# Kernel optimization log

Measured on AMD Instinct MI355X. Metric: run time of the kernel, lower is better.

The kernel has to match this reference:

```python
import jax, jax.numpy as jnp
import numpy as np

T, B, IN_DIM, H = 512, 64, 1024, 1024

def setup_inputs() -> dict:
    key = jax.random.key(0)
    kx, kwx, kwh = jax.random.split(key, 3)
    x = jax.random.normal(kx, (T, B, IN_DIM), dtype=jnp.float32)
    # lecun_normal: std = 1/sqrt(fan_in)
    W_x = jax.random.normal(kwx, (IN_DIM, 4 * H), dtype=jnp.float32) / np.sqrt(IN_DIM)
    W_h = jax.random.normal(kwh, (H, 4 * H), dtype=jnp.float32) / np.sqrt(H)
    b = jnp.zeros((4 * H,), dtype=jnp.float32)
    return {"x": x, "W_x": W_x, "W_h": W_h, "b": b}

def reference(x, W_x, W_h, b):
    Tn, Bn, _ = x.shape
    Hn = W_h.shape[0]
    h0 = jnp.zeros((Bn, Hn), dtype=x.dtype)
    c0 = jnp.zeros((Bn, Hn), dtype=x.dtype)

    def step(carry, xt):
        h, c = carry
        gates = xt @ W_x + h @ W_h + b  # [B, 4H]
        i, f, g, o = jnp.split(gates, 4, axis=-1)
        i = jax.nn.sigmoid(i)
        f = jax.nn.sigmoid(f)
        o = jax.nn.sigmoid(o)
        g = jnp.tanh(g)
        c_new = f * c + i * g
        h_new = o * jnp.tanh(c_new)
        return (h_new, c_new), h_new

    (hT, cT), hs = jax.lax.scan(step, (h0, c0), x)
    return hs, (hT, cT)
```

## Files before the change

kernel.cpp:

```cpp
#include <hip/hip_runtime.h>

typedef unsigned short u16;
typedef unsigned int u32;
typedef unsigned long long u64;
typedef float f32x4 __attribute__((ext_vector_type(4)));
typedef __bf16 bf16x8 __attribute__((ext_vector_type(8)));
typedef u16 u16x8 __attribute__((ext_vector_type(8)));
typedef u32 u32x4 __attribute__((ext_vector_type(4)));

#define T_STEPS 512
#define BATCH 64
#define HDIM 1024
#define GDIM 4096
#define HS_ELEMS (33554432u)
#define XP_STEP 262144

__device__ __forceinline__ u16 f2bf(float f) {
  union { float f; u32 u; } v; v.f = f;
  u32 r = v.u + 0x7fffu + ((v.u >> 16) & 1u);
  return (u16)(r >> 16);
}
__device__ __forceinline__ float bf2f(u16 b) {
  union { u32 u; float f; } v; v.u = ((u32)b) << 16;
  return v.f;
}
__device__ __forceinline__ float sigm(float x) { return 1.f / (1.f + __expf(-x)); }
__device__ __forceinline__ float tanh_fast(float x) { return 1.f - 2.f / (__expf(2.f * x) + 1.f); }

__device__ __forceinline__ void gload16(const void* g, void* l) {
  __builtin_amdgcn_global_load_lds(
      (const __attribute__((address_space(1))) u32*)g,
      (__attribute__((address_space(3))) u32*)l, 16, 0, 0);
}
__device__ __forceinline__ u32x4 cload16(const void* g) {
  u32x4 r;
  asm volatile("global_load_dwordx4 %0, %1, off sc0 sc1" : "=&v"(r) : "v"(g) : "memory");
  return r;
}

__global__ void transpose_w(const float* __restrict__ Wx, const float* __restrict__ Wh,
                            u16* __restrict__ WxT, u16* __restrict__ WhT) {
  __shared__ float tile[32][33];
  const float* src = blockIdx.z ? Wh : Wx;
  u16* dst = blockIdx.z ? WhT : WxT;
  const int n0 = blockIdx.x * 32, k0 = blockIdx.y * 32;
  const int tx = threadIdx.x, ty = threadIdx.y;
#pragma unroll
  for (int i = 0; i < 4; ++i)
    tile[ty + i * 8][tx] = src[(size_t)(k0 + ty + i * 8) * GDIM + n0 + tx];
  __syncthreads();
#pragma unroll
  for (int i = 0; i < 4; ++i)
    dst[(size_t)(n0 + ty + i * 8) * HDIM + k0 + tx] = f2bf(tile[tx][ty + i * 8]);
}

__global__ void convert_x(const float* __restrict__ X, u16* __restrict__ Xbf) {
  const size_t i = ((size_t)blockIdx.x * 256 + threadIdx.x) * 8;
  const float4 a = *(const float4*)&X[i];
  const float4 b = *(const float4*)&X[i + 4];
  u16x8 o;
  o[0] = f2bf(a.x); o[1] = f2bf(a.y); o[2] = f2bf(a.z); o[3] = f2bf(a.w);
  o[4] = f2bf(b.x); o[5] = f2bf(b.y); o[6] = f2bf(b.z); o[7] = f2bf(b.w);
  *(u16x8*)&Xbf[i] = o;
}

__global__ __launch_bounds__(256) void gemm_xp(
    const u16* __restrict__ Xbf, const u16* __restrict__ WxT,
    const float* __restrict__ bias, u16* __restrict__ Xp) {
  __shared__ u16 As[128 * 32];
  __shared__ u16 Bs[128 * 32];
  const int tid = threadIdx.x;
  const int lane = tid & 63, w = tid >> 6;
  const int rl = lane & 15, gq = lane >> 4, g8 = gq * 8;
  const int swz = (blockIdx.x & 7) * 1024 + (blockIdx.x >> 3);
  const int m0 = (swz >> 5) * 128, n0 = (swz & 31) * 128;
  const int rbase = (w >> 1) * 64, cbase = (w & 1) * 64;
  const int r0 = tid >> 2, c0 = (tid & 3) * 8;

  f32x4 acc[4][4] = {};
  for (int k0 = 0; k0 < 1024; k0 += 32) {
    gload16(&Xbf[(size_t)(m0 + r0) * 1024 + k0 + c0], &As[w * 512]);
    gload16(&Xbf[(size_t)(m0 + r0 + 64) * 1024 + k0 + c0], &As[2048 + w * 512]);
    gload16(&WxT[(size_t)(n0 + r0) * 1024 + k0 + c0], &Bs[w * 512]);
    gload16(&WxT[(size_t)(n0 + r0 + 64) * 1024 + k0 + c0], &Bs[2048 + w * 512]);
    __syncthreads();
    bf16x8 av[4], bv[4];
#pragma unroll
    for (int i = 0; i < 4; ++i)
      av[i] = *(const bf16x8*)&As[(rbase + i * 16 + rl) * 32 + g8];
#pragma unroll
    for (int j = 0; j < 4; ++j)
      bv[j] = *(const bf16x8*)&Bs[(cbase + j * 16 + rl) * 32 + g8];
#pragma unroll
    for (int i = 0; i < 4; ++i)
#pragma unroll
      for (int j = 0; j < 4; ++j)
        acc[i][j] = __builtin_amdgcn_mfma_f32_16x16x32_bf16(av[i], bv[j], acc[i][j], 0, 0, 0);
    __syncthreads();
  }
#pragma unroll
  for (int j = 0; j < 4; ++j) {
    const int n = n0 + cbase + j * 16 + rl;
    const float bj = bias[n];
    const int gate = n >> 10, col = n & 1023;
    const int cri = col >> 5, hcoli = col & 31;
#pragma unroll
    for (int i = 0; i < 4; ++i)
#pragma unroll
      for (int r = 0; r < 4; ++r) {
        const int m = m0 + rbase + i * 16 + gq * 4 + r;
        const int tt = m >> 6, b = m & 63;
        Xp[(size_t)tt * XP_STEP + (size_t)((b >> 4) * 32 + cri) * 2048 +
           gate * 512 + (b & 15) * 32 + hcoli] = f2bf(acc[i][j][r] + bj);
      }
  }
}

__global__ void zero_tags(u32* __restrict__ ht) {
  const u32 i = blockIdx.x * 256 + threadIdx.x;
  if (i < 131200u) ht[i] = 0;
}

__global__ __launch_bounds__(512, 1) void lstm_rec(
    const u16* __restrict__ Xp, const u16* __restrict__ WhT,
    u32* __restrict__ h_tag, u32* __restrict__ flags, float* __restrict__ out) {
  __shared__ u16 h_lds[16 * 1024];
  __shared__ float gate_lds[4][2][16][20];
  const int tid = threadIdx.x;
  const int lane = tid & 63, w = tid >> 6;
  const int rl = lane & 15, gq = lane >> 4;
  const int cr = blockIdx.x & 31, bg = blockIdx.x >> 5;
  const int g = w >> 1, c2 = w & 1;

  bf16x8 wf[32];
  {
    const size_t gcol = (size_t)(g * 1024 + cr * 32 + c2 * 16 + rl) * HDIM + gq * 8;
#pragma unroll
    for (int kk = 0; kk < 32; ++kk)
      wf[kk] = *(const bf16x8*)&WhT[gcol + kk * 32];
  }

  const int b_el = tid >> 5, hcol = tid & 31;
  const int srow = tid >> 5, s32 = tid & 31;
  const int swz_w = ((srow & 7) << 4) ^ ((srow & 1) << 6);
  const int swz_r = ((rl & 7) << 4) ^ ((rl & 1) << 6);
  float creg = 0.f, hreg = 0.f;

  const u16* xp_p = Xp + (size_t)blockIdx.x * 2048 + tid;
  float xg0 = bf2f(xp_p[0]), xg1 = bf2f(xp_p[512]),
        xg2 = bf2f(xp_p[1024]), xg3 = bf2f(xp_p[1536]);

  const u32* flagrow = flags + bg * 32 + (lane & 31);

  for (int t = 0; t < T_STEPS; ++t) {
    u16 nx0 = 0, nx1 = 0, nx2 = 0, nx3 = 0;
    if (t + 1 < T_STEPS) {
      const u16* p = xp_p + XP_STEP;
      nx0 = p[0]; nx1 = p[512]; nx2 = p[1024]; nx3 = p[1536];
    }

    f32x4 acc0 = {0.f, 0.f, 0.f, 0.f}, acc1 = {0.f, 0.f, 0.f, 0.f};
    if (t > 0) {
      const u32* hrow32 =
          h_tag + (size_t)(t & 1) * 65536 + (size_t)(bg * 16 + srow) * 1024;
      char* ldsrow = (char*)h_lds + srow * 2048;
      u32x4 v[8];
#pragma unroll
      for (int u = 0; u < 8; ++u)
        v[u] = cload16((const char*)hrow32 + 512 * u + 16 * s32);
      asm volatile("s_waitcnt vmcnt(0)" ::: "memory");
      __builtin_amdgcn_sched_barrier(0);
      u32 pend = 0u;
#pragma unroll
      for (int u = 0; u < 8; ++u) {
        const u32 w0 = v[u][0], w1 = v[u][1], w2 = v[u][2], w3 = v[u][3];
        const u64 packs = (u64)((w0 & 0xffffu) | (w1 << 16)) |
                          ((u64)((w2 & 0xffffu) | (w3 << 16)) << 32);
        *(u64*)(ldsrow + ((256 * u + 8 * s32) ^ swz_w)) = packs;
        if ((w0 >> 16) < (u32)t || (w1 >> 16) < (u32)t ||
            (w2 >> 16) < (u32)t || (w3 >> 16) < (u32)t)
          pend |= (1u << u);
      }
      if (__builtin_expect(pend != 0u, 0)) {
        for (;;) {
          u32 f = __hip_atomic_load(flagrow, __ATOMIC_RELAXED, __HIP_MEMORY_SCOPE_AGENT);
          if (__all((int)(f >= (u32)t))) break;
        }
        u32x4 r[8];
#pragma unroll
        for (int u = 0; u < 8; ++u)
          if (pend & (1u << u))
            r[u] = cload16((const char*)hrow32 + 512 * u + 16 * s32);
        asm volatile("s_waitcnt vmcnt(0)" ::: "memory");
        __builtin_amdgcn_sched_barrier(0);
#pragma unroll
        for (int u = 0; u < 8; ++u)
          if (pend & (1u << u)) {
            const u32 w0 = r[u][0], w1 = r[u][1], w2 = r[u][2], w3 = r[u][3];
            if ((w0 >> 16) >= (u32)t && (w1 >> 16) >= (u32)t &&
                (w2 >> 16) >= (u32)t && (w3 >> 16) >= (u32)t) {
              const u64 packs = (u64)((w0 & 0xffffu) | (w1 << 16)) |
                                ((u64)((w2 & 0xffffu) | (w3 << 16)) << 32);
              *(u64*)(ldsrow + ((256 * u + 8 * s32) ^ swz_w)) = packs;
              pend &= ~(1u << u);
            }
          }
        while (__builtin_expect(pend != 0u, 0)) {
          const int uu = __ffs(pend) - 1;
          const u64* h64 = (const u64*)hrow32;
          const int j0 = 64 * uu + 2 * s32;
          u64 a = __hip_atomic_load(&h64[j0], __ATOMIC_RELAXED, __HIP_MEMORY_SCOPE_AGENT);
          u64 b = __hip_atomic_load(&h64[j0 + 1], __ATOMIC_RELAXED, __HIP_MEMORY_SCOPE_AGENT);
          const u32 t0 = (u32)(a >> 16) & 0xffffu, t1 = (u32)(a >> 48);
          const u32 t2 = (u32)(b >> 16) & 0xffffu, t3 = (u32)(b >> 48);
          if (t0 >= (u32)t && t1 >= (u32)t && t2 >= (u32)t && t3 >= (u32)t) {
            const u64 packs =
                (u64)(((u32)a & 0xffffu) | (((u32)(a >> 32) & 0xffffu) << 16)) |
                ((u64)(((u32)b & 0xffffu) | (((u32)(b >> 32) & 0xffffu) << 16)) << 32);
            *(u64*)(ldsrow + ((256 * uu + 8 * s32) ^ swz_w)) = packs;
            pend &= pend - 1u;
          }
        }
      }
      __syncthreads();
      const char* hrd = (const char*)h_lds + rl * 2048;
#pragma unroll
      for (int kk = 0; kk < 32; kk += 2) {
        bf16x8 a0 = *(const bf16x8*)(hrd + ((kk * 64 + gq * 16) ^ swz_r));
        bf16x8 a1 = *(const bf16x8*)(hrd + (((kk + 1) * 64 + gq * 16) ^ swz_r));
        acc0 = __builtin_amdgcn_mfma_f32_16x16x32_bf16(a0, wf[kk], acc0, 0, 0, 0);
        acc1 = __builtin_amdgcn_mfma_f32_16x16x32_bf16(a1, wf[kk + 1], acc1, 0, 0, 0);
      }
      acc0 += acc1;
    } else {
      __syncthreads();
    }
#pragma unroll
    for (int r = 0; r < 4; ++r)
      gate_lds[g][c2][gq * 4 + r][rl] = acc0[r];
    __syncthreads();
    {
      const int cq = hcol >> 4, cl = hcol & 15;
      const float gi = gate_lds[0][cq][b_el][cl] + xg0;
      const float gf = gate_lds[1][cq][b_el][cl] + xg1;
      const float gg = gate_lds[2][cq][b_el][cl] + xg2;
      const float go = gate_lds[3][cq][b_el][cl] + xg3;
      const float iv = sigm(gi);
      const float fv = sigm(gf);
      const float gv = tanh_fast(gg);
      const float ov = sigm(go);
      creg = fv * creg + iv * gv;
      hreg = ov * tanh_fast(creg);
      const u32 wv = (u32)f2bf(hreg) | ((u32)(t + 1) << 16);
      __hip_atomic_store(
          &h_tag[(size_t)((t + 1) & 1) * 65536 + (size_t)(bg * 16 + b_el) * 1024 + cr * 32 + hcol],
          wv, __ATOMIC_RELAXED, __HIP_MEMORY_SCOPE_AGENT);
    }
    if (tid == 0)
      __hip_atomic_store(&flags[bg * 32 + cr], (u32)(t + 1), __ATOMIC_RELAXED,
                         __HIP_MEMORY_SCOPE_AGENT);
    out[((size_t)t * BATCH + bg * 16 + b_el) * HDIM + cr * 32 + hcol] = hreg;
    xg0 = bf2f(nx0); xg1 = bf2f(nx1); xg2 = bf2f(nx2); xg3 = bf2f(nx3);
    xp_p += XP_STEP;
  }
  out[(size_t)HS_ELEMS + (size_t)(bg * 16 + b_el) * HDIM + cr * 32 + hcol] = hreg;
  out[(size_t)HS_ELEMS + 65536u + (size_t)(bg * 16 + b_el) * HDIM + cr * 32 + hcol] = creg;
}

extern "C" void kernel_launch(void* const* d_in, const int* in_sizes, int n_in,
                              void* d_out, int out_size, void* d_ws, size_t ws_size,
                              hipStream_t stream) {
  const float* x = (const float*)d_in[0];
  const float* Wx = (const float*)d_in[1];
  const float* Wh = (const float*)d_in[2];
  const float* bias = (const float*)d_in[3];
  float* out = (float*)d_out;
  char* ws = (char*)d_ws;

  u16* WxT = (u16*)(ws + 0);
  u32* h_tag = (u32*)(ws + 0);
  u32* flags = (u32*)(ws + 524288);
  u16* WhT = (u16*)(ws + 8388608);
  u16* Xp = (u16*)(ws + 16777216);
  u16* Xbf = (u16*)d_out;

  transpose_w<<<dim3(128, 32, 2), dim3(32, 8), 0, stream>>>(Wx, Wh, WxT, WhT);
  convert_x<<<dim3(16384), dim3(256), 0, stream>>>(x, Xbf);
  gemm_xp<<<dim3(8192), dim3(256), 0, stream>>>(Xbf, WxT, bias, Xp);
  zero_tags<<<dim3(514), dim3(256), 0, stream>>>(h_tag);
  lstm_rec<<<dim3(128), dim3(512), 0, stream>>>(Xp, WhT, h_tag, flags, out);
}
```

Baseline: 2.781 ms.

## Split recurrence across twice as many blocks and poll flags before loading h

The recurrent LSTM kernel now runs 256 blocks, each handling 8 batch rows instead of 16. The Xp layout, the h_tag indexing and the flag-array zeroing are all changed to match. Each block now spin-waits on the producer flags before fetching h, using cheaper loads and escalating to a fully coherent load every eighth poll. Tagged h values are read with lower-coherence loads, and a coherent reload serves as fallback when a tag is stale. The goal is to spread per-step latency and bandwidth across more CUs, at the cost of leaving half of each 16-row MFMA tile unused and adding more consumers per flag.

Result: no change. 2.811 ms (+1.1%).

```diff
diff --git a/kernel.cpp b/kernel.cpp
--- a/kernel.cpp
+++ b/kernel.cpp
@@ -32,9 +32,24 @@
       (const __attribute__((address_space(1))) u32*)g,
       (__attribute__((address_space(3))) u32*)l, 16, 0, 0);
 }
+__device__ __forceinline__ u32x4 lload16(const void* g) {
+  u32x4 r;
+  asm volatile("global_load_dwordx4 %0, %1, off sc0" : "=&v"(r) : "v"(g) : "memory");
+  return r;
+}
 __device__ __forceinline__ u32x4 cload16(const void* g) {
   u32x4 r;
   asm volatile("global_load_dwordx4 %0, %1, off sc0 sc1" : "=&v"(r) : "v"(g) : "memory");
+  return r;
+}
+__device__ __forceinline__ u32 lload_u32(const void* g) {
+  u32 r;
+  asm volatile("global_load_dword %0, %1, off sc0" : "=&v"(r) : "v"(g) : "memory");
+  return r;
+}
+__device__ __forceinline__ u32 cload_u32(const void* g) {
+  u32 r;
+  asm volatile("global_load_dword %0, %1, off sc0 sc1" : "=&v"(r) : "v"(g) : "memory");
   return r;
 }
 
@@ -110,26 +125,26 @@
       for (int r = 0; r < 4; ++r) {
         const int m = m0 + rbase + i * 16 + gq * 4 + r;
         const int tt = m >> 6, b = m & 63;
-        Xp[(size_t)tt * XP_STEP + (size_t)((b >> 4) * 32 + cri) * 2048 +
-           gate * 512 + (b & 15) * 32 + hcoli] = f2bf(acc[i][j][r] + bj);
+        Xp[(size_t)tt * XP_STEP + (size_t)(((b >> 3) * 32) + cri) * 1024 +
+           gate * 256 + (b & 7) * 32 + hcoli] = f2bf(acc[i][j][r] + bj);
       }
   }
 }
 
 __global__ void zero_tags(u32* __restrict__ ht) {
   const u32 i = blockIdx.x * 256 + threadIdx.x;
-  if (i < 131200u) ht[i] = 0;
+  if (i < 131328u) ht[i] = 0;
 }
 
 __global__ __launch_bounds__(512, 1) void lstm_rec(
     const u16* __restrict__ Xp, const u16* __restrict__ WhT,
     u32* __restrict__ h_tag, u32* __restrict__ flags, float* __restrict__ out) {
-  __shared__ u16 h_lds[16 * 1024];
-  __shared__ float gate_lds[4][2][16][20];
+  __shared__ u16 h_lds[8 * 1024];
+  __shared__ float gate_lds[4][2][8][20];
   const int tid = threadIdx.x;
   const int lane = tid & 63, w = tid >> 6;
   const int rl = lane & 15, gq = lane >> 4;
-  const int cr = blockIdx.x & 31, bg = blockIdx.x >> 5;
+  const int bg = blockIdx.x & 7, cr = blockIdx.x >> 3;
   const int g = w >> 1, c2 = w & 1;
 
   bf16x8 wf[32];
@@ -141,14 +156,15 @@
   }
 
   const int b_el = tid >> 5, hcol = tid & 31;
-  const int srow = tid >> 5, s32 = tid & 31;
-  const int swz_w = ((srow & 7) << 4) ^ ((srow & 1) << 6);
-  const int swz_r = ((rl & 7) << 4) ^ ((rl & 1) << 6);
+  const int srow = tid >> 6, s64 = tid & 63;
+  const int swz_w = (srow << 4) ^ ((srow & 1) << 6);
+  const int rrow = rl & 7;
+  const int swz_r = (rrow << 4) ^ ((rrow & 1) << 6);
   float creg = 0.f, hreg = 0.f;
 
-  const u16* xp_p = Xp + (size_t)blockIdx.x * 2048 + tid;
-  float xg0 = bf2f(xp_p[0]), xg1 = bf2f(xp_p[512]),
-        xg2 = bf2f(xp_p[1024]), xg3 = bf2f(xp_p[1536]);
+  const u16* xp_p = Xp + (size_t)(bg * 32 + cr) * 1024 + (tid & 255);
+  float xg0 = bf2f(xp_p[0]), xg1 = bf2f(xp_p[256]),
+        xg2 = bf2f(xp_p[512]), xg3 = bf2f(xp_p[768]);
 
   const u32* flagrow = flags + bg * 32 + (lane & 31);
 
@@ -156,74 +172,74 @@
     u16 nx0 = 0, nx1 = 0, nx2 = 0, nx3 = 0;
     if (t + 1 < T_STEPS) {
       const u16* p = xp_p + XP_STEP;
-      nx0 = p[0]; nx1 = p[512]; nx2 = p[1024]; nx3 = p[1536];
+      nx0 = p[0]; nx1 = p[256]; nx2 = p[512]; nx3 = p[768];
     }
 
     f32x4 acc0 = {0.f, 0.f, 0.f, 0.f}, acc1 = {0.f, 0.f, 0.f, 0.f};
     if (t > 0) {
-      const u32* hrow32 =
-          h_tag + (size_t)(t & 1) * 65536 + (size_t)(bg * 16 + srow) * 1024;
+      {
+        u32 it = 0;
+        for (;;) {
+          u32 f = ((it & 7u) == 7u) ? cload_u32(flagrow) : lload_u32(flagrow);
+          if (__all((int)(f >= (u32)t))) break;
+          ++it;
+        }
+      }
+      const char* hrow8 = (const char*)h_tag + (size_t)(t & 1) * 262144 +
+                          (size_t)(bg * 8 + srow) * 4096;
       char* ldsrow = (char*)h_lds + srow * 2048;
-      u32x4 v[8];
-#pragma unroll
-      for (int u = 0; u < 8; ++u)
-        v[u] = cload16((const char*)hrow32 + 512 * u + 16 * s32);
+      u32x4 v[4];
+#pragma unroll
+      for (int u = 0; u < 4; ++u)
+        v[u] = lload16(hrow8 + (s64 + 64 * u) * 16);
       asm volatile("s_waitcnt vmcnt(0)" ::: "memory");
       __builtin_amdgcn_sched_barrier(0);
       u32 pend = 0u;
 #pragma unroll
-      for (int u = 0; u < 8; ++u) {
+      for (int u = 0; u < 4; ++u) {
         const u32 w0 = v[u][0], w1 = v[u][1], w2 = v[u][2], w3 = v[u][3];
         const u64 packs = (u64)((w0 & 0xffffu) | (w1 << 16)) |
                           ((u64)((w2 & 0xffffu) | (w3 << 16)) << 32);
-        *(u64*)(ldsrow + ((256 * u + 8 * s32) ^ swz_w)) = packs;
+        *(u64*)(ldsrow + (((s64 + 64 * u) * 8) ^ swz_w)) = packs;
         if ((w0 >> 16) < (u32)t || (w1 >> 16) < (u32)t ||
             (w2 >> 16) < (u32)t || (w3 >> 16) < (u32)t)
           pend |= (1u << u);
       }
       if (__builtin_expect(pend != 0u, 0)) {
-        for (;;) {
-          u32 f = __hip_atomic_load(flagrow, __ATOMIC_RELAXED, __HIP_MEMORY_SCOPE_AGENT);
-          if (__all((int)(f >= (u32)t))) break;
-        }
-        u32x4 r[8];
-#pragma unroll
-        for (int u = 0; u < 8; ++u)
-          if (pend & (1u << u))
-            r[u] = cload16((const char*)hrow32 + 512 * u + 16 * s32);
+        u32x4 r[4];
+#pragma unroll
+        for (int u = 0; u < 4; ++u)
+          if (pend & (1u << u)) r[u] = cload16(hrow8 + (s64 + 64 * u) * 16);
         asm volatile("s_waitcnt vmcnt(0)" ::: "memory");
         __builtin_amdgcn_sched_barrier(0);
 #pragma unroll
-        for (int u = 0; u < 8; ++u)
+        for (int u = 0; u < 4; ++u)
           if (pend & (1u << u)) {
             const u32 w0 = r[u][0], w1 = r[u][1], w2 = r[u][2], w3 = r[u][3];
             if ((w0 >> 16) >= (u32)t && (w1 >> 16) >= (u32)t &&
                 (w2 >> 16) >= (u32)t && (w3 >> 16) >= (u32)t) {
               const u64 packs = (u64)((w0 & 0xffffu) | (w1 << 16)) |
                                 ((u64)((w2 & 0xffffu) | (w3 << 16)) << 32);
-              *(u64*)(ldsrow + ((256 * u + 8 * s32) ^ swz_w)) = packs;
+              *(u64*)(ldsrow + (((s64 + 64 * u) * 8) ^ swz_w)) = packs;
               pend &= ~(1u << u);
             }
           }
         while (__builtin_expect(pend != 0u, 0)) {
           const int uu = __ffs(pend) - 1;
-          const u64* h64 = (const u64*)hrow32;
-          const int j0 = 64 * uu + 2 * s32;
-          u64 a = __hip_atomic_load(&h64[j0], __ATOMIC_RELAXED, __HIP_MEMORY_SCOPE_AGENT);
-          u64 b = __hip_atomic_load(&h64[j0 + 1], __ATOMIC_RELAXED, __HIP_MEMORY_SCOPE_AGENT);
-          const u32 t0 = (u32)(a >> 16) & 0xffffu, t1 = (u32)(a >> 48);
-          const u32 t2 = (u32)(b >> 16) & 0xffffu, t3 = (u32)(b >> 48);
-          if (t0 >= (u32)t && t1 >= (u32)t && t2 >= (u32)t && t3 >= (u32)t) {
-            const u64 packs =
-                (u64)(((u32)a & 0xffffu) | (((u32)(a >> 32) & 0xffffu) << 16)) |
-                ((u64)(((u32)b & 0xffffu) | (((u32)(b >> 32) & 0xffffu) << 16)) << 32);
-            *(u64*)(ldsrow + ((256 * uu + 8 * s32) ^ swz_w)) = packs;
+          u32x4 q = cload16(hrow8 + (s64 + 64 * uu) * 16);
+          asm volatile("s_waitcnt vmcnt(0)" ::: "memory");
+          const u32 w0 = q[0], w1 = q[1], w2 = q[2], w3 = q[3];
+          if ((w0 >> 16) >= (u32)t && (w1 >> 16) >= (u32)t &&
+              (w2 >> 16) >= (u32)t && (w3 >> 16) >= (u32)t) {
+            const u64 packs = (u64)((w0 & 0xffffu) | (w1 << 16)) |
+                              ((u64)((w2 & 0xffffu) | (w3 << 16)) << 32);
+            *(u64*)(ldsrow + (((s64 + 64 * uu) * 8) ^ swz_w)) = packs;
             pend &= pend - 1u;
           }
         }
       }
       __syncthreads();
-      const char* hrd = (const char*)h_lds + rl * 2048;
+      const char* hrd = (const char*)h_lds + rrow * 2048;
 #pragma unroll
       for (int kk = 0; kk < 32; kk += 2) {
         bf16x8 a0 = *(const bf16x8*)(hrd + ((kk * 64 + gq * 16) ^ swz_r));
@@ -235,11 +251,13 @@
     } else {
       __syncthreads();
     }
-#pragma unroll
-    for (int r = 0; r < 4; ++r)
-      gate_lds[g][c2][gq * 4 + r][rl] = acc0[r];
+    if (gq < 2) {
+#pragma unroll
+      for (int r = 0; r < 4; ++r)
+        gate_lds[g][c2][gq * 4 + r][rl] = acc0[r];
+    }
     __syncthreads();
-    {
+    if (tid < 256) {
       const int cq = hcol >> 4, cl = hcol & 15;
       const float gi = gate_lds[0][cq][b_el][cl] + xg0;
       const float gf = gate_lds[1][cq][b_el][cl] + xg1;
@@ -253,18 +271,21 @@
       hreg = ov * tanh_fast(creg);
       const u32 wv = (u32)f2bf(hreg) | ((u32)(t + 1) << 16);
       __hip_atomic_store(
-          &h_tag[(size_t)((t + 1) & 1) * 65536 + (size_t)(bg * 16 + b_el) * 1024 + cr * 32 + hcol],
+          &h_tag[(size_t)((t + 1) & 1) * 65536 + (size_t)(bg * 8 + b_el) * 1024 + cr * 32 + hcol],
           wv, __ATOMIC_RELAXED, __HIP_MEMORY_SCOPE_AGENT);
     }
     if (tid == 0)
       __hip_atomic_store(&flags[bg * 32 + cr], (u32)(t + 1), __ATOMIC_RELAXED,
                          __HIP_MEMORY_SCOPE_AGENT);
-    out[((size_t)t * BATCH + bg * 16 + b_el) * HDIM + cr * 32 + hcol] = hreg;
+    if (tid < 256)
+      out[((size_t)t * BATCH + bg * 8 + b_el) * HDIM + cr * 32 + hcol] = hreg;
     xg0 = bf2f(nx0); xg1 = bf2f(nx1); xg2 = bf2f(nx2); xg3 = bf2f(nx3);
     xp_p += XP_STEP;
   }
-  out[(size_t)HS_ELEMS + (size_t)(bg * 16 + b_el) * HDIM + cr * 32 + hcol] = hreg;
-  out[(size_t)HS_ELEMS + 65536u + (size_t)(bg * 16 + b_el) * HDIM + cr * 32 + hcol] = creg;
+  if (tid < 256) {
+    out[(size_t)HS_ELEMS + (size_t)(bg * 8 + b_el) * HDIM + cr * 32 + hcol] = hreg;
+    out[(size_t)HS_ELEMS + 65536u + (size_t)(bg * 8 + b_el) * HDIM + cr * 32 + hcol] = creg;
+  }
 }
 
 extern "C" void kernel_launch(void* const* d_in, const int* in_sizes, int n_in,
@@ -287,6 +308,6 @@
   transpose_w<<<dim3(128, 32, 2), dim3(32, 8), 0, stream>>>(Wx, Wh, WxT, WhT);
   convert_x<<<dim3(16384), dim3(256), 0, stream>>>(x, Xbf);
   gemm_xp<<<dim3(8192), dim3(256), 0, stream>>>(Xbf, WxT, bias, Xp);
-  zero_tags<<<dim3(514), dim3(256), 0, stream>>>(h_tag);
-  lstm_rec<<<dim3(128), dim3(512), 0, stream>>>(Xp, WhT, h_tag, flags, out);
-}
+  zero_tags<<<dim3(513), dim3(256), 0, stream>>>(h_tag);
+  lstm_rec<<<dim3(256), dim3(512), 0, stream>>>(Xp, WhT, h_tag, flags, out);
+}
```

## Split h-vector exchange into two halves overlapped with MFMA, fuse prep kernels

Applied to the files above, without the earlier changes.

The recurrent kernel now waits on per-half readiness flags and loads the first half of the hidden state, runs the first half of the MFMA reduction, then loads and checks the second half. The second half's global loads are issued before the first-half MFMAs, so cross-block communication latency can overlap with compute. The three preprocessing kernels (weight transpose, x conversion, tag zeroing) are merged into one launch, and the tag buffer moves to a separate workspace region when space allows. The cost is an extra block barrier and flag poll per step, and the change relies on the flag layout matching the producers' per-half signalling.

After: 3.190 ms. +14.7%, slower.

```diff
diff --git a/kernel.cpp b/kernel.cpp
--- a/kernel.cpp
+++ b/kernel.cpp
@@ -38,30 +38,42 @@
   return r;
 }
 
-__global__ void transpose_w(const float* __restrict__ Wx, const float* __restrict__ Wh,
-                            u16* __restrict__ WxT, u16* __restrict__ WhT) {
+__global__ void prep(const float* __restrict__ Wx, const float* __restrict__ Wh,
+                     u16* __restrict__ WxT, u16* __restrict__ WhT,
+                     const float* __restrict__ X, u16* __restrict__ Xbf,
+                     u32* __restrict__ h_tag, int do_zero) {
   __shared__ float tile[32][33];
-  const float* src = blockIdx.z ? Wh : Wx;
-  u16* dst = blockIdx.z ? WhT : WxT;
-  const int n0 = blockIdx.x * 32, k0 = blockIdx.y * 32;
-  const int tx = threadIdx.x, ty = threadIdx.y;
-#pragma unroll
-  for (int i = 0; i < 4; ++i)
-    tile[ty + i * 8][tx] = src[(size_t)(k0 + ty + i * 8) * GDIM + n0 + tx];
-  __syncthreads();
-#pragma unroll
-  for (int i = 0; i < 4; ++i)
-    dst[(size_t)(n0 + ty + i * 8) * HDIM + k0 + tx] = f2bf(tile[tx][ty + i * 8]);
-}
-
-__global__ void convert_x(const float* __restrict__ X, u16* __restrict__ Xbf) {
-  const size_t i = ((size_t)blockIdx.x * 256 + threadIdx.x) * 8;
-  const float4 a = *(const float4*)&X[i];
-  const float4 b = *(const float4*)&X[i + 4];
-  u16x8 o;
-  o[0] = f2bf(a.x); o[1] = f2bf(a.y); o[2] = f2bf(a.z); o[3] = f2bf(a.w);
-  o[4] = f2bf(b.x); o[5] = f2bf(b.y); o[6] = f2bf(b.z); o[7] = f2bf(b.w);
-  *(u16x8*)&Xbf[i] = o;
+  const int b = blockIdx.x, tid = threadIdx.x;
+  if (b < 8192) {
+    const int z = b >> 12, rem = b & 4095;
+    const int n0 = (rem & 127) * 32, k0 = (rem >> 7) * 32;
+    const float* src = z ? Wh : Wx;
+    u16* dst = z ? WhT : WxT;
+    const int tx = tid & 31, ty = tid >> 5;
+#pragma unroll
+    for (int i = 0; i < 4; ++i)
+      tile[ty + i * 8][tx] = src[(size_t)(k0 + ty + i * 8) * GDIM + n0 + tx];
+    __syncthreads();
+#pragma unroll
+    for (int i = 0; i < 4; ++i)
+      dst[(size_t)(n0 + ty + i * 8) * HDIM + k0 + tx] = f2bf(tile[tx][ty + i * 8]);
+  } else if (b < 24576) {
+    const size_t i = ((size_t)(b - 8192) * 256 + tid) * 8;
+    const float4 a = *(const float4*)&X[i];
+    const float4 c = *(const float4*)&X[i + 4];
+    u16x8 o;
+    o[0] = f2bf(a.x); o[1] = f2bf(a.y); o[2] = f2bf(a.z); o[3] = f2bf(a.w);
+    o[4] = f2bf(c.x); o[5] = f2bf(c.y); o[6] = f2bf(c.z); o[7] = f2bf(c.w);
+    *(u16x8*)&Xbf[i] = o;
+  } else if (do_zero) {
+    const u32 j = (u32)(b - 24576) * 256 + tid;
+    if (j < 131328u) h_tag[j] = 0;
+  }
+}
+
+__global__ void zero_tags(u32* __restrict__ ht) {
+  const u32 i = blockIdx.x * 256 + threadIdx.x;
+  if (i < 131328u) ht[i] = 0;
 }
 
 __global__ __launch_bounds__(256) void gemm_xp(
@@ -116,11 +128,6 @@
   }
 }
 
-__global__ void zero_tags(u32* __restrict__ ht) {
-  const u32 i = blockIdx.x * 256 + threadIdx.x;
-  if (i < 131200u) ht[i] = 0;
-}
-
 __global__ __launch_bounds__(512, 1) void lstm_rec(
     const u16* __restrict__ Xp, const u16* __restrict__ WhT,
     u32* __restrict__ h_tag, u32* __restrict__ flags, float* __restrict__ out) {
@@ -150,7 +157,8 @@
   float xg0 = bf2f(xp_p[0]), xg1 = bf2f(xp_p[512]),
         xg2 = bf2f(xp_p[1024]), xg3 = bf2f(xp_p[1536]);
 
-  const u32* flagrow = flags + bg * 32 + (lane & 31);
+  const u32* flag_lo = flags + bg * 32 + (lane & 15);
+  const u32* flag_hi = flag_lo + 16;
 
   for (int t = 0; t < T_STEPS; ++t) {
     u16 nx0 = 0, nx1 = 0, nx2 = 0, nx3 = 0;
@@ -164,68 +172,94 @@
       const u32* hrow32 =
           h_tag + (size_t)(t & 1) * 65536 + (size_t)(bg * 16 + srow) * 1024;
       char* ldsrow = (char*)h_lds + srow * 2048;
-      u32x4 v[8];
-#pragma unroll
-      for (int u = 0; u < 8; ++u)
-        v[u] = cload16((const char*)hrow32 + 512 * u + 16 * s32);
-      asm volatile("s_waitcnt vmcnt(0)" ::: "memory");
-      __builtin_amdgcn_sched_barrier(0);
-      u32 pend = 0u;
-#pragma unroll
-      for (int u = 0; u < 8; ++u) {
-        const u32 w0 = v[u][0], w1 = v[u][1], w2 = v[u][2], w3 = v[u][3];
-        const u64 packs = (u64)((w0 & 0xffffu) | (w1 << 16)) |
-                          ((u64)((w2 & 0xffffu) | (w3 << 16)) << 32);
-        *(u64*)(ldsrow + ((256 * u + 8 * s32) ^ swz_w)) = packs;
-        if ((w0 >> 16) < (u32)t || (w1 >> 16) < (u32)t ||
-            (w2 >> 16) < (u32)t || (w3 >> 16) < (u32)t)
-          pend |= (1u << u);
-      }
-      if (__builtin_expect(pend != 0u, 0)) {
-        for (;;) {
-          u32 f = __hip_atomic_load(flagrow, __ATOMIC_RELAXED, __HIP_MEMORY_SCOPE_AGENT);
-          if (__all((int)(f >= (u32)t))) break;
-        }
-        u32x4 r[8];
-#pragma unroll
-        for (int u = 0; u < 8; ++u)
-          if (pend & (1u << u))
-            r[u] = cload16((const char*)hrow32 + 512 * u + 16 * s32);
+      for (;;) {
+        u32 f = __hip_atomic_load(flag_lo, __ATOMIC_RELAXED, __HIP_MEMORY_SCOPE_AGENT);
+        if (__all((int)(f >= (u32)t))) break;
+      }
+      {
+        u32x4 v[4];
+#pragma unroll
+        for (int u = 0; u < 4; ++u)
+          v[u] = cload16((const char*)hrow32 + 512 * u + 16 * s32);
         asm volatile("s_waitcnt vmcnt(0)" ::: "memory");
         __builtin_amdgcn_sched_barrier(0);
-#pragma unroll
-        for (int u = 0; u < 8; ++u)
-          if (pend & (1u << u)) {
-            const u32 w0 = r[u][0], w1 = r[u][1], w2 = r[u][2], w3 = r[u][3];
-            if ((w0 >> 16) >= (u32)t && (w1 >> 16) >= (u32)t &&
-                (w2 >> 16) >= (u32)t && (w3 >> 16) >= (u32)t) {
-              const u64 packs = (u64)((w0 & 0xffffu) | (w1 << 16)) |
-                                ((u64)((w2 & 0xffffu) | (w3 << 16)) << 32);
-              *(u64*)(ldsrow + ((256 * u + 8 * s32) ^ swz_w)) = packs;
-              pend &= ~(1u << u);
-            }
-          }
+        u32 pend = 0u;
+#pragma unroll
+        for (int u = 0; u < 4; ++u) {
+          const u32 w0 = v[u][0], w1 = v[u][1], w2 = v[u][2], w3 = v[u][3];
+          const u64 packs = (u64)((w0 & 0xffffu) | (w1 << 16)) |
+                            ((u64)((w2 & 0xffffu) | (w3 << 16)) << 32);
+          *(u64*)(ldsrow + ((256 * u + 8 * s32) ^ swz_w)) = packs;
+          if ((w0 >> 16) < (u32)t || (w1 >> 16) < (u32)t ||
+              (w2 >> 16) < (u32)t || (w3 >> 16) < (u32)t)
+            pend |= (1u << u);
+        }
         while (__builtin_expect(pend != 0u, 0)) {
           const int uu = __ffs(pend) - 1;
-          const u64* h64 = (const u64*)hrow32;
-          const int j0 = 64 * uu + 2 * s32;
-          u64 a = __hip_atomic_load(&h64[j0], __ATOMIC_RELAXED, __HIP_MEMORY_SCOPE_AGENT);
-          u64 b = __hip_atomic_load(&h64[j0 + 1], __ATOMIC_RELAXED, __HIP_MEMORY_SCOPE_AGENT);
-          const u32 t0 = (u32)(a >> 16) & 0xffffu, t1 = (u32)(a >> 48);
-          const u32 t2 = (u32)(b >> 16) & 0xffffu, t3 = (u32)(b >> 48);
-          if (t0 >= (u32)t && t1 >= (u32)t && t2 >= (u32)t && t3 >= (u32)t) {
-            const u64 packs =
-                (u64)(((u32)a & 0xffffu) | (((u32)(a >> 32) & 0xffffu) << 16)) |
-                ((u64)(((u32)b & 0xffffu) | (((u32)(b >> 32) & 0xffffu) << 16)) << 32);
+          u32x4 q = cload16((const char*)hrow32 + 512 * uu + 16 * s32);
+          asm volatile("s_waitcnt vmcnt(0)" ::: "memory");
+          const u32 w0 = q[0], w1 = q[1], w2 = q[2], w3 = q[3];
+          if ((w0 >> 16) >= (u32)t && (w1 >> 16) >= (u32)t &&
+              (w2 >> 16) >= (u32)t && (w3 >> 16) >= (u32)t) {
+            const u64 packs = (u64)((w0 & 0xffffu) | (w1 << 16)) |
+                              ((u64)((w2 & 0xffffu) | (w3 << 16)) << 32);
             *(u64*)(ldsrow + ((256 * uu + 8 * s32) ^ swz_w)) = packs;
             pend &= pend - 1u;
           }
         }
       }
-      __syncthreads();
+      for (;;) {
+        u32 f = __hip_atomic_load(flag_hi, __ATOMIC_RELAXED, __HIP_MEMORY_SCOPE_AGENT);
+        if (__all((int)(f >= (u32)t))) break;
+      }
+      u32x4 v2[4];
+#pragma unroll
+      for (int u = 0; u < 4; ++u)
+        v2[u] = cload16((const char*)hrow32 + 512 * (u + 4) + 16 * s32);
+      asm volatile("s_waitcnt lgkmcnt(0)" ::: "memory");
+      __builtin_amdgcn_sched_barrier(0);
+      __builtin_amdgcn_s_barrier();
       const char* hrd = (const char*)h_lds + rl * 2048;
 #pragma unroll
-      for (int kk = 0; kk < 32; kk += 2) {
+      for (int kk = 0; kk < 16; kk += 2) {
+        bf16x8 a0 = *(const bf16x8*)(hrd + ((kk * 64 + gq * 16) ^ swz_r));
+        bf16x8 a1 = *(const bf16x8*)(hrd + (((kk + 1) * 64 + gq * 16) ^ swz_r));
+        acc0 = __builtin_amdgcn_mfma_f32_16x16x32_bf16(a0, wf[kk], acc0, 0, 0, 0);
+        acc1 = __builtin_amdgcn_mfma_f32_16x16x32_bf16(a1, wf[kk + 1], acc1, 0, 0, 0);
+      }
+      asm volatile("s_waitcnt vmcnt(0)" ::: "memory");
+      __builtin_amdgcn_sched_barrier(0);
+      {
+        u32 pend = 0u;
+#pragma unroll
+        for (int u = 0; u < 4; ++u) {
+          const u32 w0 = v2[u][0], w1 = v2[u][1], w2 = v2[u][2], w3 = v2[u][3];
+          const u64 packs = (u64)((w0 & 0xffffu) | (w1 << 16)) |
+                            ((u64)((w2 & 0xffffu) | (w3 << 16)) << 32);
+          *(u64*)(ldsrow + ((256 * (u + 4) + 8 * s32) ^ swz_w)) = packs;
+          if ((w0 >> 16) < (u32)t || (w1 >> 16) < (u32)t ||
+              (w2 >> 16) < (u32)t || (w3 >> 16) < (u32)t)
+            pend |= (1u << u);
+        }
+        while (__builtin_expect(pend != 0u, 0)) {
+          const int uu = __ffs(pend) - 1;
+          u32x4 q = cload16((const char*)hrow32 + 512 * (uu + 4) + 16 * s32);
+          asm volatile("s_waitcnt vmcnt(0)" ::: "memory");
+          const u32 w0 = q[0], w1 = q[1], w2 = q[2], w3 = q[3];
+          if ((w0 >> 16) >= (u32)t && (w1 >> 16) >= (u32)t &&
+              (w2 >> 16) >= (u32)t && (w3 >> 16) >= (u32)t) {
+            const u64 packs = (u64)((w0 & 0xffffu) | (w1 << 16)) |
+                              ((u64)((w2 & 0xffffu) | (w3 << 16)) << 32);
+            *(u64*)(ldsrow + ((256 * (uu + 4) + 8 * s32) ^ swz_w)) = packs;
+            pend &= pend - 1u;
+          }
+        }
+      }
+      asm volatile("s_waitcnt lgkmcnt(0)" ::: "memory");
+      __builtin_amdgcn_sched_barrier(0);
+      __builtin_amdgcn_s_barrier();
+#pragma unroll
+      for (int kk = 16; kk < 32; kk += 2) {
         bf16x8 a0 = *(const bf16x8*)(hrd + ((kk * 64 + gq * 16) ^ swz_r));
         bf16x8 a1 = *(const bf16x8*)(hrd + (((kk + 1) * 64 + gq * 16) ^ swz_r));
         acc0 = __builtin_amdgcn_mfma_f32_16x16x32_bf16(a0, wf[kk], acc0, 0, 0, 0);
@@ -278,15 +312,17 @@
   char* ws = (char*)d_ws;
 
   u16* WxT = (u16*)(ws + 0);
-  u32* h_tag = (u32*)(ws + 0);
-  u32* flags = (u32*)(ws + 524288);
   u16* WhT = (u16*)(ws + 8388608);
   u16* Xp = (u16*)(ws + 16777216);
   u16* Xbf = (u16*)d_out;
 
-  transpose_w<<<dim3(128, 32, 2), dim3(32, 8), 0, stream>>>(Wx, Wh, WxT, WhT);
-  convert_x<<<dim3(16384), dim3(256), 0, stream>>>(x, Xbf);
+  const bool big = ws_size >= (size_t)(285212672 + 525312);
+  u32* h_tag = big ? (u32*)(ws + 285212672) : (u32*)ws;
+  u32* flags = h_tag + 131072;
+
+  prep<<<dim3(25089), dim3(256), 0, stream>>>(Wx, Wh, WxT, WhT, x, Xbf, h_tag,
+                                              big ? 1 : 0);
   gemm_xp<<<dim3(8192), dim3(256), 0, stream>>>(Xbf, WxT, bias, Xp);
-  zero_tags<<<dim3(514), dim3(256), 0, stream>>>(h_tag);
+  if (!big) zero_tags<<<dim3(513), dim3(256), 0, stream>>>(h_tag);
   lstm_rec<<<dim3(128), dim3(512), 0, stream>>>(Xp, WhT, h_tag, flags, out);
 }
```
